# Optimization experiments

Measured on AMD Instinct MI355X. Metric: run time of the kernel, lower is better.

The kernel has to match this reference:

```python
import jax, jax.numpy as jnp
import numpy as np

EMBED_DIM = 1024
NUM_HEADS = 16
HEAD_DIM = EMBED_DIM // NUM_HEADS
BATCH = 2
SEQ = 2048


def setup_inputs() -> dict:
    key = jax.random.key(0)
    k_x, k_wqkv, k_bqkv, k_wo, k_bo = jax.random.split(key, 5)
    scale = 1.0 / np.sqrt(EMBED_DIM)
    return {
        "x": jax.random.normal(k_x, (BATCH, SEQ, EMBED_DIM), dtype=jnp.float32),
        # torch nn.Linear stores weight as (out, in); we keep (in, out) and use x @ W
        "W_qkv": jax.random.normal(k_wqkv, (EMBED_DIM, 3 * EMBED_DIM), dtype=jnp.float32) * scale,
        "b_qkv": jax.random.normal(k_bqkv, (3 * EMBED_DIM,), dtype=jnp.float32) * scale,
        "W_out": jax.random.normal(k_wo, (EMBED_DIM, EMBED_DIM), dtype=jnp.float32) * scale,
        "b_out": jax.random.normal(k_bo, (EMBED_DIM,), dtype=jnp.float32) * scale,
    }


def reference(x, W_qkv, b_qkv, W_out, b_out):
    B, S, E = x.shape
    qkv = x @ W_qkv + b_qkv                                   # (B,S,3E)
    qkv = qkv.reshape(B, S, 3, NUM_HEADS, HEAD_DIM)
    qkv = jnp.transpose(qkv, (2, 0, 3, 1, 4))                  # (3,B,H,S,D)
    Q, K, V = qkv[0], qkv[1], qkv[2]
    scores = jnp.einsum("bhqd,bhkd->bhqk", Q, K) / np.sqrt(HEAD_DIM)
    causal = jnp.tril(jnp.ones((S, S), dtype=bool))
    scores = jnp.where(causal[None, None], scores, -jnp.inf)
    attention_weights = jax.nn.softmax(scores, axis=-1)        # (B,H,S,S)
    # dropout is identity in eval mode
    attended = jnp.einsum("bhqk,bhkd->bhqd", attention_weights, V)
    attended = jnp.transpose(attended, (0, 2, 1, 3)).reshape(B, S, E)
    output = attended @ W_out + b_out
    return output, attention_weights
```

## Files before the change

kernel.cpp:

```cpp
#include <hip/hip_runtime.h>
#include <hip/hip_bf16.h>
#include <math.h>

#define BATCH 2
#define SEQ 2048
#define EMBED 1024
#define NHEAD 16
#define QKV_N 3072
#define M_TOK 4096
#define NT_KV (SEQ / 64)
#define OUT_ELEMS ((size_t)M_TOK * EMBED)

typedef __attribute__((ext_vector_type(4))) float f32x4;
typedef __attribute__((ext_vector_type(8))) short bf16x8;

__device__ __forceinline__ short f2bf(float f) {
    __hip_bfloat16 h = __float2bfloat16(f);
    return *reinterpret_cast<short*>(&h);
}
__device__ __forceinline__ float bf2f(short s) {
    union { unsigned u; float f; } c;
    c.u = ((unsigned)(unsigned short)s) << 16;
    return c.f;
}

__device__ __forceinline__ void gld16(const void* g, void* l) {
    __builtin_amdgcn_global_load_lds(
        (const __attribute__((address_space(1))) unsigned int*)g,
        (__attribute__((address_space(3))) unsigned int*)l, 16, 0, 0);
}

__global__ __launch_bounds__(256) void cast_bf16_kernel(
    const float* __restrict__ in, short* __restrict__ out, int n4)
{
    int i = blockIdx.x * 256 + threadIdx.x;
    if (i >= n4) return;
    float4 v = ((const float4*)in)[i];
    unsigned long long pk =
        (unsigned long long)(unsigned short)f2bf(v.x)
      | ((unsigned long long)(unsigned short)f2bf(v.y) << 16)
      | ((unsigned long long)(unsigned short)f2bf(v.z) << 32)
      | ((unsigned long long)(unsigned short)f2bf(v.w) << 48);
    ((unsigned long long*)out)[i] = pk;
}

__global__ __launch_bounds__(256) void transpose_cast_kernel(
    const float* __restrict__ in, short* __restrict__ out, int R, int C)
{
    __shared__ float t[64][65];
    const int r0 = blockIdx.y * 64, c0 = blockIdx.x * 64;
    for (int i = threadIdx.x; i < 4096; i += 256) {
        int r = i >> 6, c = i & 63;
        t[r][c] = in[(size_t)(r0 + r) * C + c0 + c];
    }
    __syncthreads();
    for (int i = threadIdx.x; i < 4096; i += 256) {
        int c = i >> 6, r = i & 63;
        out[(size_t)(c0 + c) * R + r0 + r] = f2bf(t[r][c]);
    }
}

__global__ __launch_bounds__(256) void pack_v_kernel(
    const short* __restrict__ qkvb, short* __restrict__ Vp)
{
    __shared__ short tv[64][72];
    const int kt = blockIdx.x, bh = blockIdx.y;
    const int b = bh >> 4, h = bh & 15;
    const int t = threadIdx.x;
    const int row = t >> 2, cp = t & 3;
    const short* src = qkvb + (size_t)(b * SEQ + kt * 64 + row) * QKV_N
                       + 2 * EMBED + h * 64 + cp * 16;
    bf16x8 a0 = *(const bf16x8*)src;
    bf16x8 a1 = *(const bf16x8*)(src + 8);
    #pragma unroll
    for (int j = 0; j < 8; ++j) {
        tv[row][cp * 16 + j] = a0[j];
        tv[row][cp * 16 + 8 + j] = a1[j];
    }
    __syncthreads();
    const int d = row;
    short* dst = Vp + ((size_t)bh * NT_KV + kt) * 4096 + d * 64;
    bf16x8 o0, o1;
    #pragma unroll
    for (int j = 0; j < 8; ++j) {
        o0[j] = tv[cp * 16 + j][d];
        o1[j] = tv[cp * 16 + 8 + j][d];
    }
    *(bf16x8*)(dst + (((2 * cp) ^ (d & 7)) << 3)) = o0;
    *(bf16x8*)(dst + (((2 * cp + 1) ^ (d & 7)) << 3)) = o1;
}

template <bool OUT_BF16>
__global__ __launch_bounds__(256) void gemm_mfma_kernel(
    const short* __restrict__ A, const short* __restrict__ Bt,
    const float* __restrict__ bias, void* __restrict__ C,
    int M, int N, int K)
{
    __shared__ short As[128 * 32];
    __shared__ short Bs[128 * 32];
    const int tid = threadIdx.x;
    const int w = tid >> 6, lane = tid & 63;
    const int quad = lane >> 4, lc = lane & 15;
    const int wm = w & 1, wn = w >> 1;
    const int m0 = blockIdx.y * 128, n0 = blockIdx.x * 128;

    f32x4 acc[4][4] = {};

    const int srow = (lane >> 2);
    const int schk = ((lane & 3) ^ (srow & 3)) * 8;

    for (int k0 = 0; k0 < K; k0 += 32) {
        #pragma unroll
        for (int j = 0; j < 2; ++j) {
            int r = w * 32 + j * 16 + srow;
            gld16(A + ((size_t)(m0 + r) * K + k0 + schk), &As[(w * 32 + j * 16) * 32]);
            gld16(Bt + ((size_t)(n0 + r) * K + k0 + schk), &Bs[(w * 32 + j * 16) * 32]);
        }
        __syncthreads();
        bf16x8 af[4], bf[4];
        #pragma unroll
        for (int i = 0; i < 4; ++i)
            af[i] = *(const bf16x8*)&As[(wm * 64 + i * 16 + lc) * 32
                                        + ((quad ^ (lc & 3)) << 3)];
        #pragma unroll
        for (int i = 0; i < 4; ++i)
            bf[i] = *(const bf16x8*)&Bs[(wn * 64 + i * 16 + lc) * 32
                                        + ((quad ^ (lc & 3)) << 3)];
        #pragma unroll
        for (int mi = 0; mi < 4; ++mi)
            #pragma unroll
            for (int ni = 0; ni < 4; ++ni)
                acc[mi][ni] = __builtin_amdgcn_mfma_f32_16x16x32_bf16(
                    af[mi], bf[ni], acc[mi][ni], 0, 0, 0);
        __syncthreads();
    }

    #pragma unroll
    for (int mi = 0; mi < 4; ++mi) {
        int row = m0 + wm * 64 + mi * 16 + quad * 4;
        #pragma unroll
        for (int ni = 0; ni < 4; ++ni) {
            int col = n0 + wn * 64 + ni * 16 + lc;
            float bc = bias[col];
            #pragma unroll
            for (int r = 0; r < 4; ++r) {
                float v = acc[mi][ni][r] + bc;
                if (OUT_BF16)
                    ((short*)C)[(size_t)(row + r) * N + col] = f2bf(v);
                else
                    ((float*)C)[(size_t)(row + r) * N + col] = v;
            }
        }
    }
}

__global__ __launch_bounds__(256) void attn_kernel(
    const short* __restrict__ qkvb,
    const short* __restrict__ Vp,
    float* __restrict__ attw,
    short* __restrict__ attb)
{
    const int NT = NT_KV;
    const int qt = (blockIdx.y & 8) ? (NT - 1 - (int)blockIdx.x) : (int)blockIdx.x;
    const int bh = blockIdx.y;
    const int b = bh >> 4, h = bh & 15;
    const int tid = threadIdx.x;
    const int w = tid >> 6, lane = tid & 63;
    const int quad = lane >> 4, lc = lane & 15;
    const int qloc = w * 16 + quad * 4;

    __shared__ short Kb[64 * 64];
    __shared__ short Vt[64 * 64];
    __shared__ short Ps[4][16 * 64];

    const short* qptr = qkvb + (size_t)(b * SEQ + qt * 64 + w * 16 + lc) * QKV_N
                        + h * 64 + quad * 8;
    const bf16x8 qf0 = *(const bf16x8*)qptr;
    const bf16x8 qf1 = *(const bf16x8*)(qptr + 32);

    const int srow = lane >> 3;
    const int schk = ((lane & 7) ^ srow) * 8;

    float m_i[4], l_i[4];
    #pragma unroll
    for (int r = 0; r < 4; ++r) { m_i[r] = -INFINITY; l_i[r] = 0.f; }

    for (int kt = 0; kt <= qt; ++kt) {
        __syncthreads();
        #pragma unroll
        for (int j = 0; j < 2; ++j) {
            int row = w * 16 + j * 8 + srow;
            gld16(qkvb + (size_t)(b * SEQ + kt * 64 + row) * QKV_N
                       + EMBED + h * 64 + schk,
                  &Kb[(w * 16 + j * 8) * 64]);
        }
        __syncthreads();

        const bool diag = (kt == qt);
        float sv[4][4];
        #pragma unroll
        for (int ni = 0; ni < 4; ++ni) {
            const int key = ni * 16 + lc;
            f32x4 acc = {};
            bf16x8 kf0 = *(const bf16x8*)&Kb[key * 64 + ((quad ^ (key & 7)) << 3)];
            bf16x8 kf1 = *(const bf16x8*)&Kb[key * 64 + (((quad | 4) ^ (key & 7)) << 3)];
            acc = __builtin_amdgcn_mfma_f32_16x16x32_bf16(qf0, kf0, acc, 0, 0, 0);
            acc = __builtin_amdgcn_mfma_f32_16x16x32_bf16(qf1, kf1, acc, 0, 0, 0);
            #pragma unroll
            for (int r = 0; r < 4; ++r) {
                float v = acc[r] * 0.125f;
                if (diag && key > (qloc + r)) v = -INFINITY;
                sv[ni][r] = v;
            }
        }
        #pragma unroll
        for (int r = 0; r < 4; ++r) {
            float mx = fmaxf(fmaxf(sv[0][r], sv[1][r]), fmaxf(sv[2][r], sv[3][r]));
            #pragma unroll
            for (int d = 1; d <= 8; d <<= 1) mx = fmaxf(mx, __shfl_xor(mx, d, 64));
            float mn = fmaxf(m_i[r], mx);
            float s = __expf(sv[0][r] - mn) + __expf(sv[1][r] - mn)
                    + __expf(sv[2][r] - mn) + __expf(sv[3][r] - mn);
            #pragma unroll
            for (int d = 1; d <= 8; d <<= 1) s += __shfl_xor(s, d, 64);
            l_i[r] = l_i[r] * __expf(m_i[r] - mn) + s;
            m_i[r] = mn;
        }
    }

    float inv_l[4];
    #pragma unroll
    for (int r = 0; r < 4; ++r) inv_l[r] = 1.0f / l_i[r];

    f32x4 o[4] = {};
    for (int kt = 0; kt <= qt; ++kt) {
        __syncthreads();
        #pragma unroll
        for (int j = 0; j < 2; ++j) {
            int row = w * 16 + j * 8 + srow;
            gld16(qkvb + (size_t)(b * SEQ + kt * 64 + row) * QKV_N
                       + EMBED + h * 64 + schk,
                  &Kb[(w * 16 + j * 8) * 64]);
            gld16(Vp + ((size_t)bh * NT + kt) * 4096 + (w * 16 + j * 8) * 64 + lane * 8,
                  &Vt[(w * 16 + j * 8) * 64]);
        }
        __syncthreads();

        const bool diag = (kt == qt);
        short* Psw = Ps[w];
        #pragma unroll
        for (int ni = 0; ni < 4; ++ni) {
            const int key = ni * 16 + lc;
            f32x4 acc = {};
            bf16x8 kf0 = *(const bf16x8*)&Kb[key * 64 + ((quad ^ (key & 7)) << 3)];
            bf16x8 kf1 = *(const bf16x8*)&Kb[key * 64 + (((quad | 4) ^ (key & 7)) << 3)];
            acc = __builtin_amdgcn_mfma_f32_16x16x32_bf16(qf0, kf0, acc, 0, 0, 0);
            acc = __builtin_amdgcn_mfma_f32_16x16x32_bf16(qf1, kf1, acc, 0, 0, 0);
            #pragma unroll
            for (int r = 0; r < 4; ++r) {
                float v = acc[r] * 0.125f;
                bool msk = diag && key > (qloc + r);
                float p = msk ? 0.f : __expf(v - m_i[r]) * inv_l[r];
                int prow = quad * 4 + r;
                Psw[prow * 64 + (key ^ ((prow & 7) << 3))] = f2bf(p);
            }
        }
        #pragma unroll
        for (int kd = 0; kd < 2; ++kd) {
            bf16x8 pf = *(const bf16x8*)&Psw[lc * 64
                        + (((kd * 4 + quad) ^ (lc & 7)) << 3)];
            #pragma unroll
            for (int ni = 0; ni < 4; ++ni) {
                const int d = ni * 16 + lc;
                bf16x8 vf = *(const bf16x8*)&Vt[d * 64
                            + (((kd * 4 + quad) ^ (d & 7)) << 3)];
                o[ni] = __builtin_amdgcn_mfma_f32_16x16x32_bf16(pf, vf, o[ni], 0, 0, 0);
            }
        }
        {
            const int a = lane & 7;
            #pragma unroll
            for (int wb = 0; wb < 2; ++wb) {
                const int r8 = wb * 8 + srow;
                bf16x8 pv = *(const bf16x8*)&Psw[r8 * 64 + a * 8];
                const int colc = (a ^ (r8 & 7)) << 3;
                float* dst = attw + ((size_t)bh * SEQ + qt * 64 + w * 16 + r8) * SEQ
                             + kt * 64 + colc;
                f32x4 f0 = { bf2f(pv[0]), bf2f(pv[1]), bf2f(pv[2]), bf2f(pv[3]) };
                f32x4 f1 = { bf2f(pv[4]), bf2f(pv[5]), bf2f(pv[6]), bf2f(pv[7]) };
                __builtin_nontemporal_store(f0, (f32x4*)dst);
                __builtin_nontemporal_store(f1, (f32x4*)dst + 1);
            }
        }
    }

    #pragma unroll
    for (int ni = 0; ni < 4; ++ni)
        #pragma unroll
        for (int r = 0; r < 4; ++r)
            attb[(size_t)(b * SEQ + qt * 64 + qloc + r) * EMBED
                 + h * 64 + ni * 16 + lc] = f2bf(o[ni][r]);

    if (qt < NT - 1) {
        const int zc4 = (qt + 1) * 16;
        for (int r = 0; r < 64; ++r) {
            f32x4* rowp = (f32x4*)(attw + ((size_t)bh * SEQ + qt * 64 + r) * SEQ);
            f32x4 z = {};
            for (int c = zc4 + tid; c < 512; c += 256)
                __builtin_nontemporal_store(z, rowp + c);
        }
    }
}

extern "C" void kernel_launch(void* const* d_in, const int* in_sizes, int n_in,
                              void* d_out, int out_size, void* d_ws, size_t ws_size,
                              hipStream_t stream)
{
    const float* x     = (const float*)d_in[0];
    const float* W_qkv = (const float*)d_in[1];
    const float* b_qkv = (const float*)d_in[2];
    const float* W_out = (const float*)d_in[3];
    const float* b_out = (const float*)d_in[4];

    float* out  = (float*)d_out;
    float* attw = out + OUT_ELEMS;

    short* xb   = (short*)d_ws;
    short* wqt  = xb + (size_t)M_TOK * EMBED;
    short* wot  = wqt + (size_t)QKV_N * EMBED;
    short* qkvb = wot + (size_t)EMBED * EMBED;
    short* attb = qkvb + (size_t)M_TOK * QKV_N;
    short* Vp   = xb;

    cast_bf16_kernel<<<OUT_ELEMS / 4 / 256, 256, 0, stream>>>(x, xb, (int)(OUT_ELEMS / 4));
    transpose_cast_kernel<<<dim3(QKV_N / 64, EMBED / 64), 256, 0, stream>>>(W_qkv, wqt, EMBED, QKV_N);
    transpose_cast_kernel<<<dim3(EMBED / 64, EMBED / 64), 256, 0, stream>>>(W_out, wot, EMBED, EMBED);

    gemm_mfma_kernel<true><<<dim3(QKV_N / 128, M_TOK / 128), 256, 0, stream>>>(
        xb, wqt, b_qkv, qkvb, M_TOK, QKV_N, EMBED);

    pack_v_kernel<<<dim3(NT_KV, BATCH * NHEAD), 256, 0, stream>>>(qkvb, Vp);

    attn_kernel<<<dim3(NT_KV, BATCH * NHEAD), 256, 0, stream>>>(qkvb, Vp, attw, attb);

    gemm_mfma_kernel<false><<<dim3(EMBED / 128, M_TOK / 128), 256, 0, stream>>>(
        attb, wot, b_out, out, M_TOK, EMBED, EMBED);
}
```

Baseline: 772.5 us.

## Double-buffer K/V tiles in attention with prefetch and MFMA priority hints

```diff
diff --git a/kernel.cpp b/kernel.cpp
--- a/kernel.cpp
+++ b/kernel.cpp
@@ -154,7 +154,7 @@
     }
 }
 
-__global__ __launch_bounds__(256) void attn_kernel(
+__global__ __launch_bounds__(256, 4) void attn_kernel(
     const short* __restrict__ qkvb,
     const short* __restrict__ Vp,
     float* __restrict__ attw,
@@ -169,8 +169,8 @@
     const int quad = lane >> 4, lc = lane & 15;
     const int qloc = w * 16 + quad * 4;
 
-    __shared__ short Kb[64 * 64];
-    __shared__ short Vt[64 * 64];
+    __shared__ short Kb[2][64 * 64];
+    __shared__ short Vt[2][64 * 64];
     __shared__ short Ps[4][16 * 64];
 
     const short* qptr = qkvb + (size_t)(b * SEQ + qt * 64 + w * 16 + lc) * QKV_N
@@ -181,29 +181,39 @@
     const int srow = lane >> 3;
     const int schk = ((lane & 7) ^ srow) * 8;
 
+    const short* kg0 = qkvb + (size_t)(b * SEQ + w * 16 + srow) * QKV_N
+                       + EMBED + h * 64 + schk;
+    const size_t kstep = (size_t)64 * QKV_N;
+    const short* vg0 = Vp + (size_t)bh * NT * 4096 + (w * 16) * 64 + lane * 8;
+
+    auto stage_k = [&](int kt, int bi) {
+        gld16(kg0 + (size_t)kt * kstep, &Kb[bi][(w * 16) * 64]);
+        gld16(kg0 + (size_t)kt * kstep + (size_t)8 * QKV_N, &Kb[bi][(w * 16 + 8) * 64]);
+    };
+    auto stage_v = [&](int kt, int bi) {
+        gld16(vg0 + (size_t)kt * 4096, &Vt[bi][(w * 16) * 64]);
+        gld16(vg0 + (size_t)kt * 4096 + 512, &Vt[bi][(w * 16 + 8) * 64]);
+    };
+
     float m_i[4], l_i[4];
     #pragma unroll
     for (int r = 0; r < 4; ++r) { m_i[r] = -INFINITY; l_i[r] = 0.f; }
 
+    int buf = 0;
+    stage_k(0, 0);
+    __syncthreads();
     for (int kt = 0; kt <= qt; ++kt) {
-        __syncthreads();
-        #pragma unroll
-        for (int j = 0; j < 2; ++j) {
-            int row = w * 16 + j * 8 + srow;
-            gld16(qkvb + (size_t)(b * SEQ + kt * 64 + row) * QKV_N
-                       + EMBED + h * 64 + schk,
-                  &Kb[(w * 16 + j * 8) * 64]);
-        }
-        __syncthreads();
-
+        if (kt < qt) stage_k(kt + 1, buf ^ 1);
         const bool diag = (kt == qt);
+        const short* kb = Kb[buf];
         float sv[4][4];
+        __builtin_amdgcn_s_setprio(1);
         #pragma unroll
         for (int ni = 0; ni < 4; ++ni) {
             const int key = ni * 16 + lc;
             f32x4 acc = {};
-            bf16x8 kf0 = *(const bf16x8*)&Kb[key * 64 + ((quad ^ (key & 7)) << 3)];
-            bf16x8 kf1 = *(const bf16x8*)&Kb[key * 64 + (((quad | 4) ^ (key & 7)) << 3)];
+            bf16x8 kf0 = *(const bf16x8*)&kb[key * 64 + ((quad ^ (key & 7)) << 3)];
+            bf16x8 kf1 = *(const bf16x8*)&kb[key * 64 + (((quad | 4) ^ (key & 7)) << 3)];
             acc = __builtin_amdgcn_mfma_f32_16x16x32_bf16(qf0, kf0, acc, 0, 0, 0);
             acc = __builtin_amdgcn_mfma_f32_16x16x32_bf16(qf1, kf1, acc, 0, 0, 0);
             #pragma unroll
@@ -213,6 +223,7 @@
                 sv[ni][r] = v;
             }
         }
+        __builtin_amdgcn_s_setprio(0);
         #pragma unroll
         for (int r = 0; r < 4; ++r) {
             float mx = fmaxf(fmaxf(sv[0][r], sv[1][r]), fmaxf(sv[2][r], sv[3][r]));
@@ -226,6 +237,8 @@
             l_i[r] = l_i[r] * __expf(m_i[r] - mn) + s;
             m_i[r] = mn;
         }
+        __syncthreads();
+        buf ^= 1;
     }
 
     float inv_l[4];
@@ -233,29 +246,26 @@
     for (int r = 0; r < 4; ++r) inv_l[r] = 1.0f / l_i[r];
 
     f32x4 o[4] = {};
+    buf = 0;
+    stage_k(0, 0);
+    stage_v(0, 0);
+    __syncthreads();
     for (int kt = 0; kt <= qt; ++kt) {
-        __syncthreads();
-        #pragma unroll
-        for (int j = 0; j < 2; ++j) {
-            int row = w * 16 + j * 8 + srow;
-            gld16(qkvb + (size_t)(b * SEQ + kt * 64 + row) * QKV_N
-                       + EMBED + h * 64 + schk,
-                  &Kb[(w * 16 + j * 8) * 64]);
-            gld16(Vp + ((size_t)bh * NT + kt) * 4096 + (w * 16 + j * 8) * 64 + lane * 8,
-                  &Vt[(w * 16 + j * 8) * 64]);
-        }
-        __syncthreads();
-
+        if (kt < qt) { stage_k(kt + 1, buf ^ 1); stage_v(kt + 1, buf ^ 1); }
         const bool diag = (kt == qt);
+        const short* kb = Kb[buf];
+        const short* vb = Vt[buf];
         short* Psw = Ps[w];
         #pragma unroll
         for (int ni = 0; ni < 4; ++ni) {
             const int key = ni * 16 + lc;
             f32x4 acc = {};
-            bf16x8 kf0 = *(const bf16x8*)&Kb[key * 64 + ((quad ^ (key & 7)) << 3)];
-            bf16x8 kf1 = *(const bf16x8*)&Kb[key * 64 + (((quad | 4) ^ (key & 7)) << 3)];
+            bf16x8 kf0 = *(const bf16x8*)&kb[key * 64 + ((quad ^ (key & 7)) << 3)];
+            bf16x8 kf1 = *(const bf16x8*)&kb[key * 64 + (((quad | 4) ^ (key & 7)) << 3)];
+            __builtin_amdgcn_s_setprio(1);
             acc = __builtin_amdgcn_mfma_f32_16x16x32_bf16(qf0, kf0, acc, 0, 0, 0);
             acc = __builtin_amdgcn_mfma_f32_16x16x32_bf16(qf1, kf1, acc, 0, 0, 0);
+            __builtin_amdgcn_s_setprio(0);
             #pragma unroll
             for (int r = 0; r < 4; ++r) {
                 float v = acc[r] * 0.125f;
@@ -265,6 +275,7 @@
                 Psw[prow * 64 + (key ^ ((prow & 7) << 3))] = f2bf(p);
             }
         }
+        __builtin_amdgcn_s_setprio(1);
         #pragma unroll
         for (int kd = 0; kd < 2; ++kd) {
             bf16x8 pf = *(const bf16x8*)&Psw[lc * 64
@@ -272,11 +283,12 @@
             #pragma unroll
             for (int ni = 0; ni < 4; ++ni) {
                 const int d = ni * 16 + lc;
-                bf16x8 vf = *(const bf16x8*)&Vt[d * 64
+                bf16x8 vf = *(const bf16x8*)&vb[d * 64
                             + (((kd * 4 + quad) ^ (d & 7)) << 3)];
                 o[ni] = __builtin_amdgcn_mfma_f32_16x16x32_bf16(pf, vf, o[ni], 0, 0, 0);
             }
         }
+        __builtin_amdgcn_s_setprio(0);
         {
             const int a = lane & 7;
             #pragma unroll
@@ -292,6 +304,10 @@
                 __builtin_nontemporal_store(f1, (f32x4*)dst + 1);
             }
         }
+        asm volatile("s_waitcnt vmcnt(4) lgkmcnt(0)" ::: "memory");
+        __builtin_amdgcn_s_barrier();
+        __builtin_amdgcn_sched_barrier(0);
+        buf ^= 1;
     }
 
     #pragma unroll
```

After: 776.7 us. About the same (+0.5%).
